# Kernel optimization log

Hardware: AMD Instinct MI355X
Metric: run time of the kernel (lower is better)

Reference implementation:

```python
import jax, jax.numpy as jnp
import numpy as np

MG = (5, 5)          # mesh_grid_size
UP = (17, 17)        # upsample_size
IMG = (512.0, 512.0) # image_size
B = 8192
FC_OUT = MG[0] * MG[1] * 2  # 50
KH = (UP[0] - 1) // (MG[0] - 1) + 1  # 5
KW = (UP[1] - 1) // (MG[1] - 1) + 1  # 5
SH = (UP[0] - 1) // (MG[0] - 1)      # 4
SW = (UP[1] - 1) // (MG[1] - 1)      # 4
L0 = MG[0] - 1
L1 = MG[1] - 1


def _grid(h, w):
    # channel 0: x coords vary along rows (image_size[0]); channel 1: y along cols
    x_t = jnp.broadcast_to(jnp.linspace(0.0, IMG[0], h)[:, None], (h, w))
    y_t = jnp.broadcast_to(jnp.linspace(0.0, IMG[1], w)[None, :], (h, w))
    return jnp.stack([x_t, y_t], 0)  # [2, h, w]


def _unfold22(a):
    # a: [B, 2, H, W] -> [B, (H-1)*(W-1), 4, 2]; 4 = kernel positions row-major, 2 = channel
    p = jnp.stack([a[:, :, :-1, :-1], a[:, :, :-1, 1:],
                   a[:, :, 1:, :-1], a[:, :, 1:, 1:]], axis=2)  # [B,2,4,H-1,W-1]
    return p.reshape(a.shape[0], 2, 4, -1).transpose(0, 3, 2, 1)


def _persp(src, dst):
    # exact 4-point homography solve (torchgeometry.get_perspective_transform)
    x0, y0 = src[..., 0], src[..., 1]
    u, v = dst[..., 0], dst[..., 1]
    z = jnp.zeros_like(x0)
    o = jnp.ones_like(x0)
    ax = jnp.stack([x0, y0, o, z, z, z, -u * x0, -u * y0], -1)  # [N,4,8]
    ay = jnp.stack([z, z, z, x0, y0, o, -v * x0, -v * y0], -1)
    A = jnp.concatenate([ax, ay], 1)                 # [N,8,8]
    bb = jnp.concatenate([u, v], 1)[..., None]       # [N,8,1]
    h = jnp.linalg.solve(A, bb)[..., 0]              # [N,8]
    return jnp.concatenate([h, o[:, :1]], 1).reshape(-1, 3, 3)


def setup_inputs() -> dict:
    key = jax.random.key(0)
    ks = jax.random.split(key, 4)
    def lin(k, i, o):
        return jax.random.normal(k, (i, o), jnp.float32) / jnp.sqrt(i)
    return {
        "x": jax.random.normal(ks[0], (B, 1024), jnp.float32),
        "W1": lin(ks[1], 1024, 1024), "b1": jnp.zeros((1024,), jnp.float32),
        "W2": lin(ks[2], 1024, 2048), "b2": jnp.zeros((2048,), jnp.float32),
        "W3": lin(ks[3], 2048, FC_OUT), "b3": jnp.zeros((FC_OUT,), jnp.float32),
    }


def reference(x, W1, b1, W2, b2, W3, b3):
    Bn = x.shape[0]
    h = jax.nn.relu(x @ W1 + b1)
    h = jax.nn.relu(h @ W2 + b2)
    out = (h @ W3 + b3).reshape(Bn, 2, MG[0], MG[1])  # [B,2,5,5] mesh flow

    # sparse control grid and 2x2 patch corner points
    gs = _grid(MG[0], MG[1])
    src = _unfold22(jnp.broadcast_to(gs[None], (Bn, 2, MG[0], MG[1]))).reshape(-1, 4, 2)
    flow = _unfold22(out).reshape(-1, 4, 2)
    M = _persp(src, src + flow)  # [B*16, 3, 3]

    # dense grid and its unfold2 (kernel KHxKW, stride SHxSW) patch points
    gd = _grid(UP[0], UP[1])  # [2, 17, 17]
    gi = (np.arange(L0) * SH)[:, None, None, None] + np.arange(KH)[None, None, :, None]
    gj = (np.arange(L1) * SW)[None, :, None, None] + np.arange(KW)[None, None, None, :]
    I, J = np.broadcast_arrays(gi, gj)  # [L0,L1,KH,KW]
    pts = gd[:, I, J].transpose(1, 2, 3, 4, 0).reshape(1, L0 * L1, KH * KW, 2)
    pts = jnp.broadcast_to(pts, (Bn, L0 * L1, KH * KW, 2)).reshape(Bn * L0 * L1, KH * KW, 2)

    # transform_points: homogeneous warp + perspective divide
    ph = jnp.concatenate([pts, jnp.ones(pts.shape[:-1] + (1,), pts.dtype)], -1)
    oh = jnp.einsum('nij,npj->npi', M, ph)
    warped = oh[..., :2] / oh[..., 2:3]
    warped = warped.reshape(Bn, L0, L1, KH, KW, 2)

    # Fold: scatter-accumulate overlapping patches
    fold = jnp.zeros((Bn, 2, UP[0], UP[1]), x.dtype)
    for i in range(L0):
        for j in range(L1):
            blk = warped[:, i, j].transpose(0, 3, 1, 2)  # [B,2,KH,KW]
            fold = fold.at[:, :, i * SH:i * SH + KH, j * SW:j * SW + KW].add(blk)

    # boundary rescaling exactly as the torch code: only the 5x5 crossing points
    idx = np.arange(0, UP[0], MG[0] - 1)
    X, Y = np.meshgrid(idx, idx, indexing='xy')
    fold = fold.at[:, :, X, Y].multiply(0.5)
    for (a, b) in ((0, 0), (0, UP[1] - 1), (UP[0] - 1, UP[1] - 1), (UP[0] - 1, 0)):
        fold = fold.at[:, :, a, b].multiply(2.0)

    return fold - gd[None]  # upsampled mesh flow [B,2,17,17]
```

## Files before the change

kernel.cpp:

```cpp
#include <hip/hip_runtime.h>

typedef __bf16 bf16x8 __attribute__((ext_vector_type(8)));
typedef float f32x4 __attribute__((ext_vector_type(4)));

__device__ __forceinline__ unsigned short f2bf(float f) {
  unsigned int u = __builtin_bit_cast(unsigned int, f);
  unsigned int r = (u + 0x7fffu + ((u >> 16) & 1u)) >> 16;
  return (unsigned short)r;
}

__device__ __forceinline__ float bf2f(unsigned short u) {
  unsigned int v = ((unsigned int)u) << 16;
  return __builtin_bit_cast(float, v);
}

__device__ __forceinline__ void load16_lds(const unsigned short* g, unsigned short* l) {
  __builtin_amdgcn_global_load_lds(
      (const __attribute__((address_space(1))) void*)g,
      (__attribute__((address_space(3))) void*)l, 16, 0, 0);
}


__global__ __launch_bounds__(256) void prepass(
    const float* __restrict__ x, const float* __restrict__ W1,
    const float* __restrict__ W2, const float* __restrict__ W3,
    unsigned short* __restrict__ xbf, unsigned short* __restrict__ w1t,
    unsigned short* __restrict__ w2t, unsigned short* __restrict__ w3t) {
  __shared__ float tile[32][33];
  const int bid = blockIdx.x;
  const int t = threadIdx.x;
  if (bid < 2048) {
    for (int i = bid * 256 + t; i < 2097152; i += 2048 * 256) {
      float4 f = ((const float4*)x)[i];
      uint2 o;
      o.x = (unsigned)f2bf(f.x) | ((unsigned)f2bf(f.y) << 16);
      o.y = (unsigned)f2bf(f.z) | ((unsigned)f2bf(f.w) << 16);
      ((uint2*)xbf)[i] = o;
    }
  } else if (bid < 3072) {
    int ti = bid - 2048;
    int n0 = (ti & 31) * 32, k0 = (ti >> 5) * 32;
    int tx = t & 31, ty = t >> 5;
    #pragma unroll
    for (int r = 0; r < 32; r += 8)
      tile[ty + r][tx] = W1[(size_t)(k0 + ty + r) * 1024 + n0 + tx];
    __syncthreads();
    #pragma unroll
    for (int r = 0; r < 32; r += 8)
      w1t[(size_t)(n0 + ty + r) * 1024 + k0 + tx] = f2bf(tile[tx][ty + r]);
  } else if (bid < 5120) {
    int ti = bid - 3072;
    int n0 = (ti & 63) * 32, k0 = (ti >> 6) * 32;
    int tx = t & 31, ty = t >> 5;
    #pragma unroll
    for (int r = 0; r < 32; r += 8)
      tile[ty + r][tx] = W2[(size_t)(k0 + ty + r) * 2048 + n0 + tx];
    __syncthreads();
    #pragma unroll
    for (int r = 0; r < 32; r += 8)
      w2t[(size_t)(n0 + ty + r) * 1024 + k0 + tx] = f2bf(tile[tx][ty + r]);
  } else {
    int idx = (bid - 5120) * 256 + t;
    int n = idx >> 11, k = idx & 2047;
    w3t[idx] = f2bf((n < 50) ? W3[(size_t)k * 50 + n] : 0.f);
  }
}


__global__ __launch_bounds__(256) void gemm1_f128(
    const unsigned short* __restrict__ A,
    const unsigned short* __restrict__ Bt,
    const float* __restrict__ bias,
    unsigned short* __restrict__ C) {
  constexpr int K = 1024, N = 1024;
  __shared__ __align__(16) unsigned short smem[2 * 128 * 64];
  unsigned short* As = smem;
  unsigned short* Bs = smem + 128 * 64;
  const int t = threadIdx.x;
  const int m0 = blockIdx.x * 128;
  const int n0 = blockIdx.y * 128;
  const int lane = t & 63, wv = t >> 6;
  const int l16 = lane & 15, quad = lane >> 4;
  const int wm = (wv >> 1) * 64, wn = (wv & 1) * 64;

  const int srow = t >> 3;
  const int scol = ((t & 7) ^ (srow & 7)) * 8;
  const unsigned short* Ag0 = A + (size_t)(m0 + srow) * K + scol;
  const unsigned short* Bg0 = Bt + (size_t)(n0 + srow) * K + scol;
  unsigned short* AsW = As + wv * 8 * 64;
  unsigned short* BsW = Bs + wv * 8 * 64;

  f32x4 acc[4][4] = {};

  for (int k0 = 0; k0 < K; k0 += 64) {
    #pragma unroll
    for (int r = 0; r < 4; ++r) {
      load16_lds(Ag0 + (size_t)(r * 32) * K + k0, AsW + r * 32 * 64);
      load16_lds(Bg0 + (size_t)(r * 32) * K + k0, BsW + r * 32 * 64);
    }
    __syncthreads();
    #pragma unroll
    for (int half = 0; half < 2; ++half) {
      bf16x8 af[4], bfr[4];
      #pragma unroll
      for (int mi = 0; mi < 4; ++mi) {
        int row = wm + mi * 16 + l16;
        int pb = (half * 4 + quad) ^ (row & 7);
        af[mi] = *(const bf16x8*)&As[row * 64 + pb * 8];
      }
      #pragma unroll
      for (int ni = 0; ni < 4; ++ni) {
        int row = wn + ni * 16 + l16;
        int pb = (half * 4 + quad) ^ (row & 7);
        bfr[ni] = *(const bf16x8*)&Bs[row * 64 + pb * 8];
      }
      #pragma unroll
      for (int mi = 0; mi < 4; ++mi)
        #pragma unroll
        for (int ni = 0; ni < 4; ++ni)
          acc[mi][ni] = __builtin_amdgcn_mfma_f32_16x16x32_bf16(
              af[mi], bfr[ni], acc[mi][ni], 0, 0, 0);
    }
    __syncthreads();
  }

  unsigned short* Cs = smem;
  #pragma unroll
  for (int ni = 0; ni < 4; ++ni) {
    int col = wn + ni * 16 + l16;
    float bv = bias[n0 + col];
    #pragma unroll
    for (int mi = 0; mi < 4; ++mi) {
      #pragma unroll
      for (int r = 0; r < 4; ++r) {
        int row = wm + mi * 16 + quad * 4 + r;
        Cs[row * 128 + col] = f2bf(fmaxf(acc[mi][ni][r] + bv, 0.f));
      }
    }
  }
  __syncthreads();
  #pragma unroll
  for (int j = 0; j < 8; ++j) {
    int idx = j * 256 + t;
    int row = idx >> 4;
    int cc = (idx & 15) * 8;
    *(uint4*)&C[(size_t)(m0 + row) * N + n0 + cc] = *(const uint4*)&Cs[row * 128 + cc];
  }
}


__global__ __launch_bounds__(256) void gemm2_fused(
    const unsigned short* __restrict__ A,
    const unsigned short* __restrict__ Bt,
    const float* __restrict__ bias,
    const unsigned short* __restrict__ W3t,
    unsigned short* __restrict__ part) {
  constexpr int K = 1024;
  __shared__ __align__(16) unsigned short smem[2 * 128 * 64];
  unsigned short* As = smem;
  unsigned short* Bs = smem + 128 * 64;
  const int t = threadIdx.x;
  const int m0 = blockIdx.x * 128;
  const int n0 = blockIdx.y * 128;
  const int lane = t & 63, wv = t >> 6;
  const int l16 = lane & 15, quad = lane >> 4;
  const int wm = (wv >> 1) * 64, wn = (wv & 1) * 64;

  const int srow = t >> 3;
  const int scol = ((t & 7) ^ (srow & 7)) * 8;
  const unsigned short* Ag0 = A + (size_t)(m0 + srow) * K + scol;
  const unsigned short* Bg0 = Bt + (size_t)(n0 + srow) * K + scol;
  unsigned short* AsW = As + wv * 8 * 64;
  unsigned short* BsW = Bs + wv * 8 * 64;

  bf16x8 bq[4][4];
  #pragma unroll
  for (int ks = 0; ks < 4; ++ks)
    #pragma unroll
    for (int nt = 0; nt < 4; ++nt)
      bq[ks][nt] = *(const bf16x8*)&W3t[(size_t)(nt * 16 + l16) * 2048 +
                                        n0 + ks * 32 + quad * 8];
  float bv4[4];
  #pragma unroll
  for (int ni = 0; ni < 4; ++ni) bv4[ni] = bias[n0 + wn + ni * 16 + l16];

  f32x4 acc[4][4] = {};

  for (int k0 = 0; k0 < K; k0 += 64) {
    #pragma unroll
    for (int r = 0; r < 4; ++r) {
      load16_lds(Ag0 + (size_t)(r * 32) * K + k0, AsW + r * 32 * 64);
      load16_lds(Bg0 + (size_t)(r * 32) * K + k0, BsW + r * 32 * 64);
    }
    __syncthreads();
    #pragma unroll
    for (int half = 0; half < 2; ++half) {
      bf16x8 af[4], bfr[4];
      #pragma unroll
      for (int mi = 0; mi < 4; ++mi) {
        int row = wm + mi * 16 + l16;
        int pb = (half * 4 + quad) ^ (row & 7);
        af[mi] = *(const bf16x8*)&As[row * 64 + pb * 8];
      }
      #pragma unroll
      for (int ni = 0; ni < 4; ++ni) {
        int row = wn + ni * 16 + l16;
        int pb = (half * 4 + quad) ^ (row & 7);
        bfr[ni] = *(const bf16x8*)&Bs[row * 64 + pb * 8];
      }
      #pragma unroll
      for (int mi = 0; mi < 4; ++mi)
        #pragma unroll
        for (int ni = 0; ni < 4; ++ni)
          acc[mi][ni] = __builtin_amdgcn_mfma_f32_16x16x32_bf16(
              af[mi], bfr[ni], acc[mi][ni], 0, 0, 0);
    }
    __syncthreads();
  }

  unsigned short* Cs = smem;
  #pragma unroll
  for (int ni = 0; ni < 4; ++ni) {
    int col = wn + ni * 16 + l16;
    float bv = bv4[ni];
    int cb = col >> 3, cw = col & 7;
    #pragma unroll
    for (int mi = 0; mi < 4; ++mi) {
      #pragma unroll
      for (int r = 0; r < 4; ++r) {
        int row = wm + mi * 16 + quad * 4 + r;
        int pb = cb ^ (row & 15);
        Cs[row * 128 + pb * 8 + cw] = f2bf(fmaxf(acc[mi][ni][r] + bv, 0.f));
      }
    }
  }
  __syncthreads();

  f32x4 acc2[2][4] = {};
  #pragma unroll
  for (int ks = 0; ks < 4; ++ks) {
    bf16x8 af2[2];
    #pragma unroll
    for (int mt = 0; mt < 2; ++mt) {
      int row = wv * 32 + mt * 16 + l16;
      int pb = (ks * 4 + quad) ^ (row & 15);
      af2[mt] = *(const bf16x8*)&Cs[row * 128 + pb * 8];
    }
    #pragma unroll
    for (int mt = 0; mt < 2; ++mt)
      #pragma unroll
      for (int nt = 0; nt < 4; ++nt)
        acc2[mt][nt] = __builtin_amdgcn_mfma_f32_16x16x32_bf16(
            af2[mt], bq[ks][nt], acc2[mt][nt], 0, 0, 0);
  }

  unsigned short* pb3 = part + (size_t)blockIdx.y * 8192 * 64;
  #pragma unroll
  for (int mt = 0; mt < 2; ++mt) {
    #pragma unroll
    for (int nt = 0; nt < 4; ++nt) {
      int col = nt * 16 + l16;
      #pragma unroll
      for (int r = 0; r < 4; ++r) {
        int row = m0 + wv * 32 + mt * 16 + quad * 4 + r;
        pb3[(size_t)row * 64 + col] = f2bf(acc2[mt][nt][r]);
      }
    }
  }
}


__global__ __launch_bounds__(256) void geom_reduce(
    const unsigned short* __restrict__ part, const float* __restrict__ b3,
    float* __restrict__ outp) {
  __shared__ float s_out3[16 * 64];
  __shared__ float fold[16 * 578];
  const int t = threadIdx.x;
  const int bbase = blockIdx.x * 16;

  for (int i = t; i < 16 * 578; i += 256) fold[i] = 0.f;
  for (int i = t; i < 1024; i += 256) {
    int m = i >> 6, n = i & 63;
    size_t idx = (size_t)(bbase + m) * 64 + n;
    float v = 0.f;
    #pragma unroll
    for (int z = 0; z < 16; ++z) v += bf2f(part[idx + (size_t)z * 8192 * 64]);
    s_out3[i] = v + ((n < 50) ? b3[n] : 0.f);
  }
  __syncthreads();

  {
    const int bl = t >> 4;
    const int p = t & 15;
    const int pi = p >> 2, pj = p & 3;
    const float* o = &s_out3[bl * 64];

    float u00 = 128.f * pi       + o[pi * 5 + pj];
    float v00 = 128.f * pj       + o[25 + pi * 5 + pj];
    float u01 = 128.f * pi       + o[pi * 5 + pj + 1];
    float v01 = 128.f * (pj + 1) + o[25 + pi * 5 + pj + 1];
    float u10 = 128.f * (pi + 1) + o[(pi + 1) * 5 + pj];
    float v10 = 128.f * pj       + o[25 + (pi + 1) * 5 + pj];
    float u11 = 128.f * (pi + 1) + o[(pi + 1) * 5 + pj + 1];
    float v11 = 128.f * (pj + 1) + o[25 + (pi + 1) * 5 + pj + 1];

    float sx = u00 - u10 + u11 - u01;
    float sy = v00 - v10 + v11 - v01;
    float dx1 = u10 - u11, dx2 = u01 - u11;
    float dy1 = v10 - v11, dy2 = v01 - v11;
    float rden = 1.f / (dx1 * dy2 - dx2 * dy1);
    float g = (sx * dy2 - dx2 * sy) * rden;
    float h = (dx1 * sy - sx * dy1) * rden;
    float a = u10 - u00 + g * u10;
    float b = u01 - u00 + h * u01;
    float c = u00;
    float d = v10 - v00 + g * v10;
    float e = v01 - v00 + h * v01;
    float f = v00;

    #pragma unroll
    for (int ai = 0; ai < 5; ++ai) {
      #pragma unroll
      for (int bi = 0; bi < 5; ++bi) {
        float s = 0.25f * ai, tt = 0.25f * bi;
        float rw = 1.f / (g * s + h * tt + 1.f);
        float xx = (a * s + b * tt + c) * rw;
        float yy = (d * s + e * tt + f) * rw;
        int gi = pi * 4 + ai, gj = pj * 4 + bi;
        atomicAdd(&fold[(bl * 2 + 0) * 289 + gi * 17 + gj], xx);
        atomicAdd(&fold[(bl * 2 + 1) * 289 + gi * 17 + gj], yy);
      }
    }
  }
  __syncthreads();

  for (int i = t; i < 16 * 578; i += 256) {
    int blb = i / 578;
    int rem = i - blb * 578;
    int ch = rem / 289;
    int ij = rem - ch * 289;
    int gi = ij / 17, gj = ij - gi * 17;
    float val = fold[i];
    if ((gi % 4 == 0) && (gj % 4 == 0)) val *= 0.5f;
    if ((gi == 0 || gi == 16) && (gj == 0 || gj == 16)) val *= 2.f;
    val -= (ch == 0) ? 32.f * gi : 32.f * gj;
    outp[(size_t)(bbase + blb) * 578 + rem] = val;
  }
}


extern "C" void kernel_launch(void* const* d_in, const int* in_sizes, int n_in,
                              void* d_out, int out_size, void* d_ws, size_t ws_size,
                              hipStream_t stream) {
  const float* x  = (const float*)d_in[0];
  const float* W1 = (const float*)d_in[1];
  const float* b1 = (const float*)d_in[2];
  const float* W2 = (const float*)d_in[3];
  const float* b2 = (const float*)d_in[4];
  const float* W3 = (const float*)d_in[5];
  const float* b3 = (const float*)d_in[6];
  float* outp = (float*)d_out;

  char* ws = (char*)d_ws;
  unsigned short* xbf = (unsigned short*)ws;
  unsigned short* w1t = (unsigned short*)(ws + (size_t)16 * 1024 * 1024);
  unsigned short* part = (unsigned short*)ws;
  unsigned short* w2t = (unsigned short*)(ws + (size_t)34 * 1024 * 1024);
  unsigned short* w3t = (unsigned short*)(ws + (size_t)38 * 1024 * 1024);
  unsigned short* h1  = (unsigned short*)(ws + (size_t)38 * 1024 * 1024 + 512 * 1024);

  prepass<<<5632, 256, 0, stream>>>(x, W1, W2, W3, xbf, w1t, w2t, w3t);

  gemm1_f128<<<dim3(64, 8), 256, 0, stream>>>(xbf, w1t, b1, h1);
  gemm2_fused<<<dim3(64, 16), 256, 0, stream>>>(h1, w2t, b2, w3t, part);
  geom_reduce<<<512, 256, 0, stream>>>(part, b3, outp);
}
```

Before: 207.1 us.

## Rewrite both GEMMs as 8-wave double-buffered pipelines with larger tiles

Both GEMM kernels move to 512-thread blocks with double-buffered LDS. Global-to-LDS loads for the next k-tile are interleaved with MFMA phases, using raw barriers, explicit waitcnt and setprio. GEMM2 grows to 256x256 tiles, so the fused W3 projection yields 8 partial slices instead of 16 and geom_reduce sums fewer partials. The aim is to hide memory latency and cut redundant operand loads. In exchange it uses more LDS and registers per block and leaves fewer blocks to fill the CUs.

```diff
diff --git a/kernel.cpp b/kernel.cpp
--- a/kernel.cpp
+++ b/kernel.cpp
@@ -18,6 +18,20 @@
   __builtin_amdgcn_global_load_lds(
       (const __attribute__((address_space(1))) void*)g,
       (__attribute__((address_space(3))) void*)l, 16, 0, 0);
+}
+
+__device__ __forceinline__ void wait_vm0() {
+  asm volatile("s_waitcnt vmcnt(0)" ::: "memory");
+  __builtin_amdgcn_sched_barrier(0);
+}
+__device__ __forceinline__ void wait_lgkm0() {
+  asm volatile("s_waitcnt lgkmcnt(0)" ::: "memory");
+  __builtin_amdgcn_sched_barrier(0);
+}
+__device__ __forceinline__ void barrier_raw() {
+  __builtin_amdgcn_sched_barrier(0);
+  __builtin_amdgcn_s_barrier();
+  __builtin_amdgcn_sched_barrier(0);
 }
 
 
@@ -67,184 +81,303 @@
 }
 
 
-__global__ __launch_bounds__(256) void gemm1_f128(
+__global__ __launch_bounds__(512, 2) void gemm1_8p(
     const unsigned short* __restrict__ A,
     const unsigned short* __restrict__ Bt,
     const float* __restrict__ bias,
     unsigned short* __restrict__ C) {
-  constexpr int K = 1024, N = 1024;
-  __shared__ __align__(16) unsigned short smem[2 * 128 * 64];
-  unsigned short* As = smem;
-  unsigned short* Bs = smem + 128 * 64;
+  constexpr int K = 1024, N = 1024, NT = 16;
+  constexpr int AEL = 256 * 64;
+  constexpr int BEL = 128 * 64;
+  constexpr int BUF = AEL + BEL;
+  __shared__ __align__(16) unsigned short smem[2 * BUF];
   const int t = threadIdx.x;
-  const int m0 = blockIdx.x * 128;
+  const int m0 = blockIdx.x * 256;
   const int n0 = blockIdx.y * 128;
   const int lane = t & 63, wv = t >> 6;
   const int l16 = lane & 15, quad = lane >> 4;
-  const int wm = (wv >> 1) * 64, wn = (wv & 1) * 64;
+  const int wr = wv >> 1, wc = wv & 1;
+  const int rb = wr * 64, cb = wc * 64;
 
   const int srow = t >> 3;
-  const int scol = ((t & 7) ^ (srow & 7)) * 8;
-  const unsigned short* Ag0 = A + (size_t)(m0 + srow) * K + scol;
-  const unsigned short* Bg0 = Bt + (size_t)(n0 + srow) * K + scol;
-  unsigned short* AsW = As + wv * 8 * 64;
-  unsigned short* BsW = Bs + wv * 8 * 64;
+  const int sg = ((t & 7) ^ (srow & 7)) * 8;
+  const unsigned short* Ag0 = A + (size_t)(m0 + srow) * K + sg;
+  const unsigned short* Bg0 = Bt + (size_t)(n0 + srow) * K + sg;
+  const int ldsO = wv * 8 * 64;
 
   f32x4 acc[4][4] = {};
 
-  for (int k0 = 0; k0 < K; k0 += 64) {
-    #pragma unroll
-    for (int r = 0; r < 4; ++r) {
-      load16_lds(Ag0 + (size_t)(r * 32) * K + k0, AsW + r * 32 * 64);
-      load16_lds(Bg0 + (size_t)(r * 32) * K + k0, BsW + r * 32 * 64);
-    }
-    __syncthreads();
-    #pragma unroll
-    for (int half = 0; half < 2; ++half) {
-      bf16x8 af[4], bfr[4];
-      #pragma unroll
-      for (int mi = 0; mi < 4; ++mi) {
-        int row = wm + mi * 16 + l16;
-        int pb = (half * 4 + quad) ^ (row & 7);
-        af[mi] = *(const bf16x8*)&As[row * 64 + pb * 8];
+  #pragma unroll
+  for (int r = 0; r < 4; ++r)
+    load16_lds(Ag0 + (size_t)(r * 64) * K, &smem[r * 4096 + ldsO]);
+  #pragma unroll
+  for (int r = 0; r < 2; ++r)
+    load16_lds(Bg0 + (size_t)(r * 64) * K, &smem[AEL + r * 4096 + ldsO]);
+
+  for (int kt = 0; kt < NT; ++kt) {
+    unsigned short* Ls = &smem[(kt & 1) * BUF];
+    unsigned short* Ln = &smem[((kt + 1) & 1) * BUF];
+    const unsigned short* An = Ag0 + (size_t)(kt + 1) * 64;
+    const unsigned short* Bn = Bg0 + (size_t)(kt + 1) * 64;
+    const bool dost = (kt + 1 < NT);
+
+    wait_vm0();
+    barrier_raw();
+
+    bf16x8 af[4], bfr[4];
+
+    #pragma unroll
+    for (int ni = 0; ni < 4; ++ni) {
+      int row = cb + ni * 16 + l16;
+      bfr[ni] = *(const bf16x8*)&Ls[AEL + row * 64 + (quad ^ (row & 7)) * 8];
+    }
+    #pragma unroll
+    for (int mi = 0; mi < 4; ++mi) {
+      int row = rb + mi * 16 + l16;
+      af[mi] = *(const bf16x8*)&Ls[row * 64 + (quad ^ (row & 7)) * 8];
+    }
+    if (dost) {
+      load16_lds(An, &Ln[ldsO]);
+      load16_lds(An + (size_t)64 * K, &Ln[4096 + ldsO]);
+      load16_lds(An + (size_t)128 * K, &Ln[8192 + ldsO]);
+    }
+    barrier_raw();
+    wait_lgkm0();
+    __builtin_amdgcn_s_setprio(1);
+    #pragma unroll
+    for (int mi = 0; mi < 4; ++mi)
+      #pragma unroll
+      for (int ni = 0; ni < 4; ++ni)
+        acc[mi][ni] = __builtin_amdgcn_mfma_f32_16x16x32_bf16(
+            af[mi], bfr[ni], acc[mi][ni], 0, 0, 0);
+    __builtin_amdgcn_s_setprio(0);
+    barrier_raw();
+
+    #pragma unroll
+    for (int ni = 0; ni < 4; ++ni) {
+      int row = cb + ni * 16 + l16;
+      bfr[ni] = *(const bf16x8*)&Ls[AEL + row * 64 + ((4 + quad) ^ (row & 7)) * 8];
+    }
+    #pragma unroll
+    for (int mi = 0; mi < 4; ++mi) {
+      int row = rb + mi * 16 + l16;
+      af[mi] = *(const bf16x8*)&Ls[row * 64 + ((4 + quad) ^ (row & 7)) * 8];
+    }
+    if (dost) {
+      load16_lds(An + (size_t)192 * K, &Ln[12288 + ldsO]);
+      load16_lds(Bn, &Ln[AEL + ldsO]);
+      load16_lds(Bn + (size_t)64 * K, &Ln[AEL + 4096 + ldsO]);
+    }
+    barrier_raw();
+    wait_lgkm0();
+    __builtin_amdgcn_s_setprio(1);
+    #pragma unroll
+    for (int mi = 0; mi < 4; ++mi)
+      #pragma unroll
+      for (int ni = 0; ni < 4; ++ni)
+        acc[mi][ni] = __builtin_amdgcn_mfma_f32_16x16x32_bf16(
+            af[mi], bfr[ni], acc[mi][ni], 0, 0, 0);
+    __builtin_amdgcn_s_setprio(0);
+    barrier_raw();
+  }
+
+  unsigned short* Cs = smem;
+  float bv[4];
+  #pragma unroll
+  for (int ni = 0; ni < 4; ++ni) bv[ni] = bias[n0 + cb + ni * 16 + l16];
+  #pragma unroll
+  for (int mi = 0; mi < 4; ++mi)
+    #pragma unroll
+    for (int ni = 0; ni < 4; ++ni)
+      #pragma unroll
+      for (int r = 0; r < 4; ++r) {
+        int row = rb + mi * 16 + quad * 4 + r;
+        int col = cb + ni * 16 + l16;
+        int pb = (col >> 3) ^ (row & 15);
+        Cs[row * 128 + pb * 8 + (col & 7)] = f2bf(fmaxf(acc[mi][ni][r] + bv[ni], 0.f));
       }
-      #pragma unroll
-      for (int ni = 0; ni < 4; ++ni) {
-        int row = wn + ni * 16 + l16;
-        int pb = (half * 4 + quad) ^ (row & 7);
-        bfr[ni] = *(const bf16x8*)&Bs[row * 64 + pb * 8];
-      }
-      #pragma unroll
-      for (int mi = 0; mi < 4; ++mi)
-        #pragma unroll
-        for (int ni = 0; ni < 4; ++ni)
-          acc[mi][ni] = __builtin_amdgcn_mfma_f32_16x16x32_bf16(
-              af[mi], bfr[ni], acc[mi][ni], 0, 0, 0);
-    }
-    __syncthreads();
-  }
-
-  unsigned short* Cs = smem;
-  #pragma unroll
-  for (int ni = 0; ni < 4; ++ni) {
-    int col = wn + ni * 16 + l16;
-    float bv = bias[n0 + col];
-    #pragma unroll
-    for (int mi = 0; mi < 4; ++mi) {
-      #pragma unroll
-      for (int r = 0; r < 4; ++r) {
-        int row = wm + mi * 16 + quad * 4 + r;
-        Cs[row * 128 + col] = f2bf(fmaxf(acc[mi][ni][r] + bv, 0.f));
-      }
-    }
-  }
   __syncthreads();
   #pragma unroll
   for (int j = 0; j < 8; ++j) {
-    int idx = j * 256 + t;
-    int row = idx >> 4;
-    int cc = (idx & 15) * 8;
-    *(uint4*)&C[(size_t)(m0 + row) * N + n0 + cc] = *(const uint4*)&Cs[row * 128 + cc];
-  }
-}
-
-
-__global__ __launch_bounds__(256) void gemm2_fused(
+    int idx = j * 512 + t;
+    int row = idx >> 4, cg = idx & 15;
+    int pb = cg ^ (row & 15);
+    *(uint4*)&C[(size_t)(m0 + row) * N + n0 + cg * 8] =
+        *(const uint4*)&Cs[row * 128 + pb * 8];
+  }
+}
+
+
+__global__ __launch_bounds__(512, 2) void gemm2_8p(
     const unsigned short* __restrict__ A,
     const unsigned short* __restrict__ Bt,
     const float* __restrict__ bias,
     const unsigned short* __restrict__ W3t,
     unsigned short* __restrict__ part) {
-  constexpr int K = 1024;
-  __shared__ __align__(16) unsigned short smem[2 * 128 * 64];
-  unsigned short* As = smem;
-  unsigned short* Bs = smem + 128 * 64;
+  constexpr int K = 1024, NT = 16;
+  constexpr int AEL = 256 * 64;
+  constexpr int BUF = 2 * AEL;
+  __shared__ __align__(16) unsigned short smem[2 * BUF];
   const int t = threadIdx.x;
-  const int m0 = blockIdx.x * 128;
-  const int n0 = blockIdx.y * 128;
+  const int m0 = blockIdx.x * 256;
+  const int n0 = blockIdx.y * 256;
   const int lane = t & 63, wv = t >> 6;
   const int l16 = lane & 15, quad = lane >> 4;
-  const int wm = (wv >> 1) * 64, wn = (wv & 1) * 64;
+  const int wr = wv >> 2, wc = wv & 3;
+  const int rb = wr * 128, cb = wc * 64;
 
   const int srow = t >> 3;
-  const int scol = ((t & 7) ^ (srow & 7)) * 8;
-  const unsigned short* Ag0 = A + (size_t)(m0 + srow) * K + scol;
-  const unsigned short* Bg0 = Bt + (size_t)(n0 + srow) * K + scol;
-  unsigned short* AsW = As + wv * 8 * 64;
-  unsigned short* BsW = Bs + wv * 8 * 64;
-
-  bf16x8 bq[4][4];
-  #pragma unroll
-  for (int ks = 0; ks < 4; ++ks)
+  const int sg = ((t & 7) ^ (srow & 7)) * 8;
+  const unsigned short* Ag0 = A + (size_t)(m0 + srow) * K + sg;
+  const unsigned short* Bg0 = Bt + (size_t)(n0 + srow) * K + sg;
+  const int ldsO = wv * 8 * 64;
+
+  f32x4 acc[8][4] = {};
+
+  #pragma unroll
+  for (int r = 0; r < 4; ++r) {
+    load16_lds(Ag0 + (size_t)(r * 64) * K, &smem[r * 4096 + ldsO]);
+    load16_lds(Bg0 + (size_t)(r * 64) * K, &smem[AEL + r * 4096 + ldsO]);
+  }
+
+  for (int kt = 0; kt < NT; ++kt) {
+    unsigned short* Ls = &smem[(kt & 1) * BUF];
+    unsigned short* Ln = &smem[((kt + 1) & 1) * BUF];
+    const unsigned short* An = Ag0 + (size_t)(kt + 1) * 64;
+    const unsigned short* Bn = Bg0 + (size_t)(kt + 1) * 64;
+    const bool dost = (kt + 1 < NT);
+
+    wait_vm0();
+    barrier_raw();
+
+    bf16x8 af[4], bfr[4];
+
+    #pragma unroll
+    for (int ni = 0; ni < 4; ++ni) {
+      int row = cb + ni * 16 + l16;
+      bfr[ni] = *(const bf16x8*)&Ls[AEL + row * 64 + (quad ^ (row & 7)) * 8];
+    }
+    #pragma unroll
+    for (int mi = 0; mi < 4; ++mi) {
+      int row = rb + mi * 16 + l16;
+      af[mi] = *(const bf16x8*)&Ls[row * 64 + (quad ^ (row & 7)) * 8];
+    }
+    if (dost) {
+      load16_lds(An, &Ln[ldsO]);
+      load16_lds(An + (size_t)64 * K, &Ln[4096 + ldsO]);
+      load16_lds(An + (size_t)128 * K, &Ln[8192 + ldsO]);
+    }
+    barrier_raw();
+    wait_lgkm0();
+    __builtin_amdgcn_s_setprio(1);
+    #pragma unroll
+    for (int mi = 0; mi < 4; ++mi)
+      #pragma unroll
+      for (int ni = 0; ni < 4; ++ni)
+        acc[mi][ni] = __builtin_amdgcn_mfma_f32_16x16x32_bf16(
+            af[mi], bfr[ni], acc[mi][ni], 0, 0, 0);
+    __builtin_amdgcn_s_setprio(0);
+    barrier_raw();
+
+    #pragma unroll
+    for (int mi = 0; mi < 4; ++mi) {
+      int row = rb + 64 + mi * 16 + l16;
+      af[mi] = *(const bf16x8*)&Ls[row * 64 + (quad ^ (row & 7)) * 8];
+    }
+    if (dost) {
+      load16_lds(An + (size_t)192 * K, &Ln[12288 + ldsO]);
+      load16_lds(Bn, &Ln[AEL + ldsO]);
+      load16_lds(Bn + (size_t)64 * K, &Ln[AEL + 4096 + ldsO]);
+    }
+    barrier_raw();
+    wait_lgkm0();
+    __builtin_amdgcn_s_setprio(1);
+    #pragma unroll
+    for (int mi = 0; mi < 4; ++mi)
+      #pragma unroll
+      for (int ni = 0; ni < 4; ++ni)
+        acc[4 + mi][ni] = __builtin_amdgcn_mfma_f32_16x16x32_bf16(
+            af[mi], bfr[ni], acc[4 + mi][ni], 0, 0, 0);
+    __builtin_amdgcn_s_setprio(0);
+    barrier_raw();
+
+    #pragma unroll
+    for (int ni = 0; ni < 4; ++ni) {
+      int row = cb + ni * 16 + l16;
+      bfr[ni] = *(const bf16x8*)&Ls[AEL + row * 64 + ((4 + quad) ^ (row & 7)) * 8];
+    }
+    #pragma unroll
+    for (int mi = 0; mi < 4; ++mi) {
+      int row = rb + 64 + mi * 16 + l16;
+      af[mi] = *(const bf16x8*)&Ls[row * 64 + ((4 + quad) ^ (row & 7)) * 8];
+    }
+    if (dost) {
+      load16_lds(Bn + (size_t)128 * K, &Ln[AEL + 8192 + ldsO]);
+      load16_lds(Bn + (size_t)192 * K, &Ln[AEL + 12288 + ldsO]);
+    }
+    barrier_raw();
+    wait_lgkm0();
+    __builtin_amdgcn_s_setprio(1);
+    #pragma unroll
+    for (int mi = 0; mi < 4; ++mi)
+      #pragma unroll
+      for (int ni = 0; ni < 4; ++ni)
+        acc[4 + mi][ni] = __builtin_amdgcn_mfma_f32_16x16x32_bf16(
+            af[mi], bfr[ni], acc[4 + mi][ni], 0, 0, 0);
+    __builtin_amdgcn_s_setprio(0);
+    barrier_raw();
+
+    #pragma unroll
+    for (int mi = 0; mi < 4; ++mi) {
+      int row = rb + mi * 16 + l16;
+      af[mi] = *(const bf16x8*)&Ls[row * 64 + ((4 + quad) ^ (row & 7)) * 8];
+    }
+    barrier_raw();
+    wait_lgkm0();
+    __builtin_amdgcn_s_setprio(1);
+    #pragma unroll
+    for (int mi = 0; mi < 4; ++mi)
+      #pragma unroll
+      for (int ni = 0; ni < 4; ++ni)
+        acc[mi][ni] = __builtin_amdgcn_mfma_f32_16x16x32_bf16(
+            af[mi], bfr[ni], acc[mi][ni], 0, 0, 0);
+    __builtin_amdgcn_s_setprio(0);
+    barrier_raw();
+  }
+
+  unsigned short* Cs = smem;
+  float bv[4];
+  #pragma unroll
+  for (int ni = 0; ni < 4; ++ni) bv[ni] = bias[n0 + cb + ni * 16 + l16];
+  #pragma unroll
+  for (int mi = 0; mi < 8; ++mi)
+    #pragma unroll
+    for (int ni = 0; ni < 4; ++ni)
+      #pragma unroll
+      for (int r = 0; r < 4; ++r) {
+        int row = rb + mi * 16 + quad * 4 + r;
+        int col = cb + ni * 16 + l16;
+        int pb = (col >> 3) ^ (row & 31);
+        Cs[row * 256 + pb * 8 + (col & 7)] = f2bf(fmaxf(acc[mi][ni][r] + bv[ni], 0.f));
+      }
+  __syncthreads();
+
+  bf16x8 bq[8][4];
+  #pragma unroll
+  for (int ks = 0; ks < 8; ++ks)
     #pragma unroll
     for (int nt = 0; nt < 4; ++nt)
       bq[ks][nt] = *(const bf16x8*)&W3t[(size_t)(nt * 16 + l16) * 2048 +
                                         n0 + ks * 32 + quad * 8];
-  float bv4[4];
-  #pragma unroll
-  for (int ni = 0; ni < 4; ++ni) bv4[ni] = bias[n0 + wn + ni * 16 + l16];
-
-  f32x4 acc[4][4] = {};
-
-  for (int k0 = 0; k0 < K; k0 += 64) {
-    #pragma unroll
-    for (int r = 0; r < 4; ++r) {
-      load16_lds(Ag0 + (size_t)(r * 32) * K + k0, AsW + r * 32 * 64);
-      load16_lds(Bg0 + (size_t)(r * 32) * K + k0, BsW + r * 32 * 64);
-    }
-    __syncthreads();
-    #pragma unroll
-    for (int half = 0; half < 2; ++half) {
-      bf16x8 af[4], bfr[4];
-      #pragma unroll
-      for (int mi = 0; mi < 4; ++mi) {
-        int row = wm + mi * 16 + l16;
-        int pb = (half * 4 + quad) ^ (row & 7);
-        af[mi] = *(const bf16x8*)&As[row * 64 + pb * 8];
-      }
-      #pragma unroll
-      for (int ni = 0; ni < 4; ++ni) {
-        int row = wn + ni * 16 + l16;
-        int pb = (half * 4 + quad) ^ (row & 7);
-        bfr[ni] = *(const bf16x8*)&Bs[row * 64 + pb * 8];
-      }
-      #pragma unroll
-      for (int mi = 0; mi < 4; ++mi)
-        #pragma unroll
-        for (int ni = 0; ni < 4; ++ni)
-          acc[mi][ni] = __builtin_amdgcn_mfma_f32_16x16x32_bf16(
-              af[mi], bfr[ni], acc[mi][ni], 0, 0, 0);
-    }
-    __syncthreads();
-  }
-
-  unsigned short* Cs = smem;
-  #pragma unroll
-  for (int ni = 0; ni < 4; ++ni) {
-    int col = wn + ni * 16 + l16;
-    float bv = bv4[ni];
-    int cb = col >> 3, cw = col & 7;
-    #pragma unroll
-    for (int mi = 0; mi < 4; ++mi) {
-      #pragma unroll
-      for (int r = 0; r < 4; ++r) {
-        int row = wm + mi * 16 + quad * 4 + r;
-        int pb = cb ^ (row & 15);
-        Cs[row * 128 + pb * 8 + cw] = f2bf(fmaxf(acc[mi][ni][r] + bv, 0.f));
-      }
-    }
-  }
-  __syncthreads();
-
   f32x4 acc2[2][4] = {};
   #pragma unroll
-  for (int ks = 0; ks < 4; ++ks) {
+  for (int ks = 0; ks < 8; ++ks) {
     bf16x8 af2[2];
     #pragma unroll
     for (int mt = 0; mt < 2; ++mt) {
       int row = wv * 32 + mt * 16 + l16;
-      int pb = (ks * 4 + quad) ^ (row & 15);
-      af2[mt] = *(const bf16x8*)&Cs[row * 128 + pb * 8];
+      int pb = (ks * 4 + quad) ^ (row & 31);
+      af2[mt] = *(const bf16x8*)&Cs[row * 256 + pb * 8];
     }
     #pragma unroll
     for (int mt = 0; mt < 2; ++mt)
@@ -254,19 +387,18 @@
             af2[mt], bq[ks][nt], acc2[mt][nt], 0, 0, 0);
   }
 
-  unsigned short* pb3 = part + (size_t)blockIdx.y * 8192 * 64;
-  #pragma unroll
-  for (int mt = 0; mt < 2; ++mt) {
+  unsigned short* pp = part + (size_t)blockIdx.y * 8192 * 64;
+  #pragma unroll
+  for (int mt = 0; mt < 2; ++mt)
     #pragma unroll
     for (int nt = 0; nt < 4; ++nt) {
       int col = nt * 16 + l16;
       #pragma unroll
       for (int r = 0; r < 4; ++r) {
         int row = m0 + wv * 32 + mt * 16 + quad * 4 + r;
-        pb3[(size_t)row * 64 + col] = f2bf(acc2[mt][nt][r]);
+        pp[(size_t)row * 64 + col] = f2bf(acc2[mt][nt][r]);
       }
     }
-  }
 }
 
 
@@ -284,7 +416,7 @@
     size_t idx = (size_t)(bbase + m) * 64 + n;
     float v = 0.f;
     #pragma unroll
-    for (int z = 0; z < 16; ++z) v += bf2f(part[idx + (size_t)z * 8192 * 64]);
+    for (int z = 0; z < 8; ++z) v += bf2f(part[idx + (size_t)z * 8192 * 64]);
     s_out3[i] = v + ((n < 50) ? b3[n] : 0.f);
   }
   __syncthreads();
@@ -371,7 +503,7 @@
 
   prepass<<<5632, 256, 0, stream>>>(x, W1, W2, W3, xbf, w1t, w2t, w3t);
 
-  gemm1_f128<<<dim3(64, 8), 256, 0, stream>>>(xbf, w1t, b1, h1);
-  gemm2_fused<<<dim3(64, 16), 256, 0, stream>>>(h1, w2t, b2, w3t, part);
+  gemm1_8p<<<dim3(32, 8), 512, 0, stream>>>(xbf, w1t, b1, h1);
+  gemm2_8p<<<dim3(32, 8), 512, 0, stream>>>(h1, w2t, b2, w3t, part);
   geom_reduce<<<512, 256, 0, stream>>>(part, b3, outp);
 }
```

Result: faster. 201.2 us (-2.9%).
